# Kernel tuning notes

Measured on AMD Instinct MI355X. Metric: run time of the kernel, lower is better.

The kernel has to match this reference:

```python
import jax, jax.numpy as jnp
import numpy as np

H = 2048      # hidden_size
I = 4096      # intermediate_size
N = 128       # ssm state_size
HEADS = 64
P = 64        # head_dim
K = 4         # conv kernel
CHUNK = 256
DT_MIN, DT_MAX = 0.0, 100.0
EPS = 1e-5


def segsum(x):
    # x: (..., T) -> (..., T, T) with out[i, j] = sum_{k=j+1..i} x[k], -inf above diag
    T = x.shape[-1]
    cs = jnp.cumsum(x, axis=-1)
    d = cs[..., :, None] - cs[..., None, :]
    mask = jnp.tril(jnp.ones((T, T), dtype=bool))
    return jnp.where(mask, d, -jnp.inf)


def setup_inputs() -> dict:
    key = jax.random.key(0)
    ks = jax.random.split(key, 8)
    return {
        "hidden_states": jax.random.normal(ks[0], (2, 4096, H), jnp.float32),
        "in_proj_w": jax.random.normal(ks[1], (2 * (I + N) + HEADS, H), jnp.float32) * 0.02,
        "conv_w": jax.random.normal(ks[2], (I + 2 * N, 1, K), jnp.float32) * 0.2,
        "conv_b": jax.random.normal(ks[3], (I + 2 * N,), jnp.float32) * 0.02,
        "dt_bias": jax.random.uniform(ks[4], (HEADS,), jnp.float32),
        "A_log": jnp.log(jax.random.uniform(ks[5], (HEADS,), jnp.float32, 1.0, 16.0)),
        "D": jnp.ones((HEADS,), jnp.float32),
        "norm_w": jnp.ones((I,), jnp.float32),
        "out_proj_w": jax.random.normal(ks[6], (H, I), jnp.float32) * 0.02,
    }


def reference(hidden_states, in_proj_w, conv_w, conv_b, dt_bias, A_log, D, norm_w, out_proj_w):
    b, l, _ = hidden_states.shape
    # in_proj -> [z (I), xBC (I+2N), dt (HEADS)]  (d_mlp == 0 with these dims)
    zxbcdt = hidden_states @ in_proj_w.T
    z, xBC, dt = jnp.split(zxbcdt, [I, I + (I + 2 * N)], axis=-1)

    # causal depthwise conv1d + SiLU
    conv = jax.lax.conv_general_dilated(
        xBC.transpose(0, 2, 1), conv_w, (1,), [(K - 1, 0)],
        dimension_numbers=("NCH", "OIH", "NCH"), feature_group_count=I + 2 * N)
    xBC = jax.nn.silu((conv + conv_b[None, :, None]).transpose(0, 2, 1))
    x, B, C = jnp.split(xBC, [I, I + N], axis=-1)

    A = -jnp.exp(A_log)                                        # (h,)
    dt = jnp.clip(jax.nn.softplus(dt + dt_bias), DT_MIN, DT_MAX)  # (b,l,h)

    # SSD chunked scan (groups = 1 for B/C)
    X = x.reshape(b, l, HEADS, P) * dt[..., None]              # x * dt
    Adt = dt * A                                               # (b,l,h)
    c = l // CHUNK
    Xc = X.reshape(b, c, CHUNK, HEADS, P)
    Bc = B.reshape(b, c, CHUNK, N)
    Cc = C.reshape(b, c, CHUNK, N)
    Ac = Adt.reshape(b, c, CHUNK, HEADS).transpose(0, 3, 1, 2)  # (b,h,c,cl)
    A_cum = jnp.cumsum(Ac, axis=-1)

    # intra-chunk (diagonal) contribution
    L = jnp.exp(segsum(Ac))                                    # (b,h,c,cl,cl)
    Y_diag = jnp.einsum("bcln,bcsn,bhcls,bcshp->bclhp", Cc, Bc, L, Xc)

    # chunk states and inter-chunk recurrence
    decay_states = jnp.exp(A_cum[..., -1:] - A_cum)            # (b,h,c,cl)
    states = jnp.einsum("bcln,bhcl,bclhp->bchpn", Bc, decay_states, Xc)
    states = jnp.concatenate([jnp.zeros_like(states[:, :1]), states], axis=1)
    chunk_A = jnp.pad(A_cum[..., -1], ((0, 0), (0, 0), (1, 0)))  # (b,h,c+1)
    decay_chunk = jnp.exp(segsum(chunk_A))                     # (b,h,c+1,c+1)
    new_states = jnp.einsum("bhzc,bchpn->bzhpn", decay_chunk, states)
    prev_states = new_states[:, :-1]                           # (b,c,h,p,n)

    Y_off = jnp.einsum("bcln,bchpn,bhcl->bclhp", Cc, prev_states, jnp.exp(A_cum))
    y = (Y_diag + Y_off).reshape(b, l, HEADS, P)
    y = y + x.reshape(b, l, HEADS, P) * D[None, None, :, None]  # skip (D term)
    y = y.reshape(b, l, I)

    # gated RMSNorm (norm_before_gate=True): normalize, gate by silu(z), scale
    yf = y.astype(jnp.float32)
    yf = yf * jax.lax.rsqrt(jnp.mean(yf * yf, axis=-1, keepdims=True) + EPS)
    yf = yf * jax.nn.silu(z.astype(jnp.float32))
    y = (norm_w * yf).astype(hidden_states.dtype)

    return y @ out_proj_w.T
```

## Files before the change

### kernel.cpp

```cpp
#include <hip/hip_runtime.h>

typedef unsigned short u16;
typedef __attribute__((ext_vector_type(8))) short bfx8;
typedef __attribute__((ext_vector_type(4))) float f32x4;
typedef __attribute__((ext_vector_type(4))) unsigned short u16x4;

__device__ __forceinline__ float bf2f(u16 u){ return __builtin_bit_cast(float, (unsigned)u << 16); }
__device__ __forceinline__ u16 f2bf(float f){
  unsigned u = __builtin_bit_cast(unsigned, f);
  return (u16)((u + 0x7fffu + ((u >> 16) & 1u)) >> 16);
}

__device__ __forceinline__ void gload_lds16(const void* g, void* l){
  __builtin_amdgcn_global_load_lds((const __attribute__((address_space(1))) void*)g,
                                   (__attribute__((address_space(3))) void*)l, 16, 0, 0);
}

__global__ __launch_bounds__(256) void cvt_kernel(const float* __restrict__ in, u16* __restrict__ out, int n4){
  int i = blockIdx.x * 256 + threadIdx.x;
  if (i >= n4) return;
  f32x4 v = *(const f32x4*)&in[(long)i * 4];
  u16x4 o = { f2bf(v[0]), f2bf(v[1]), f2bf(v[2]), f2bf(v[3]) };
  *(u16x4*)&out[(long)i * 4] = o;
}

template<int F32OUT>
__global__ __launch_bounds__(512, 2)
void gemm256(const u16* __restrict__ A, const u16* __restrict__ W,
             void* __restrict__ out0, void* __restrict__ out1,
             int K, int ld0, int ld1, int nsplit)
{
  __shared__ __align__(16) u16 SA[2][16384];
  __shared__ __align__(16) u16 SB[2][16384];
  const int tid = threadIdx.x;
  const int wid = tid >> 6, lane = tid & 63;
  const int wr = wid >> 2, wc = wid & 3;
  const int bm = blockIdx.x, bn = blockIdx.y;
  const int rr = lane & 15, kg = lane >> 4;
  const int NT = K >> 6;

  const int srow = tid >> 3;
  const int ssw = ((tid & 7) * 16) ^ ((srow & 7) << 4);
  const u16* gA = A + ((long)bm * 256 + srow) * K + (ssw >> 1);
  const u16* gB = W + ((long)bn * 256 + srow) * K + (ssw >> 1);
  const long r64 = (long)64 * K;
  const int dst = tid * 8;

#define STAGE_A(t, ht) { const u16* s_ = gA + (long)(ht) * 2 * r64 + ((t) << 6); \
    gload_lds16(s_,       &SA[(t) & 1][(ht) * 8192 + dst]); \
    gload_lds16(s_ + r64, &SA[(t) & 1][(ht) * 8192 + 4096 + dst]); }
#define STAGE_B(t, ht) { const u16* s_ = gB + (long)(ht) * 2 * r64 + ((t) << 6); \
    gload_lds16(s_,       &SB[(t) & 1][(ht) * 8192 + dst]); \
    gload_lds16(s_ + r64, &SB[(t) & 1][(ht) * 8192 + 4096 + dst]); }

  const int swr = (rr & 7) << 4;
  const int ca0 = ((kg * 16) ^ swr) >> 1;
  const int ca1 = ((64 + kg * 16) ^ swr) >> 1;
  int bA[8], bB[4];
#pragma unroll
  for (int j = 0; j < 8; j++) bA[j] = ((2 * j + wr) * 16 + rr) * 64;
#pragma unroll
  for (int i = 0; i < 4; i++) bB[i] = ((4 * i + wc) * 16 + rr) * 64;

  f32x4 acc[8][4] = {};

  STAGE_A(0, 0); STAGE_A(0, 1); STAGE_B(0, 0); STAGE_B(0, 1);
  if (NT > 1) STAGE_A(1, 0);
  asm volatile("s_waitcnt vmcnt(2)" ::: "memory");
  asm volatile("s_barrier" ::: "memory");

  for (int u = 0; u < NT; ++u){
    const int p = u & 1;
    bfx8 bf[4][2];
#pragma unroll
    for (int k = 0; k < 4; ++k){
      bfx8 af[2][2];
#pragma unroll
      for (int jj = 0; jj < 2; jj++){
        const int base = bA[2 * k + jj];
        af[jj][0] = *(const bfx8*)&SA[p][base + ca0];
        af[jj][1] = *(const bfx8*)&SA[p][base + ca1];
      }
      if (k == 0){
#pragma unroll
        for (int i = 0; i < 4; i++){
          bf[i][0] = *(const bfx8*)&SB[p][bB[i] + ca0];
          bf[i][1] = *(const bfx8*)&SB[p][bB[i] + ca1];
        }
        if (u + 1 < NT) { STAGE_B(u + 1, 0); STAGE_B(u + 1, 1); }
      }
      else if (k == 1) { if (u + 1 < NT) STAGE_A(u + 1, 1); }
      else if (k == 3) {
        if (u + 2 < NT)      { STAGE_A(u + 2, 0); asm volatile("s_waitcnt vmcnt(2)" ::: "memory"); }
        else if (u + 1 < NT) { asm volatile("s_waitcnt vmcnt(0)" ::: "memory"); }
      }
      asm volatile("s_barrier" ::: "memory");
      __builtin_amdgcn_s_setprio(1);
#pragma unroll
      for (int jj = 0; jj < 2; jj++)
#pragma unroll
        for (int i = 0; i < 4; i++){
          acc[2 * k + jj][i] = __builtin_amdgcn_mfma_f32_16x16x32_bf16(af[jj][0], bf[i][0], acc[2 * k + jj][i], 0, 0, 0);
          acc[2 * k + jj][i] = __builtin_amdgcn_mfma_f32_16x16x32_bf16(af[jj][1], bf[i][1], acc[2 * k + jj][i], 0, 0, 0);
        }
      __builtin_amdgcn_s_setprio(0);
    }
  }
#undef STAGE_A
#undef STAGE_B

  int bn2 = bn; void* op = out0; int ldo = ld0;
  if (bn >= nsplit){ bn2 = bn - nsplit; op = out1; ldo = ld1; }
  const int r4b = (lane >> 4) * 4;
#pragma unroll
  for (int j = 0; j < 8; j++)
#pragma unroll
    for (int i = 0; i < 4; i++)
#pragma unroll
      for (int r4 = 0; r4 < 4; r4++){
        long row = (long)bm * 256 + (2 * j + wr) * 16 + r4b + r4;
        long col = (long)bn2 * 256 + (4 * i + wc) * 16 + rr;
        long idx = row * ldo + col;
        if (F32OUT) ((float*)op)[idx] = acc[j][i][r4];
        else        ((u16*)op)[idx]  = f2bf(acc[j][i][r4]);
      }
}

__global__ __launch_bounds__(256) void dt_kernel(const float* __restrict__ hs, const float* __restrict__ w,
                                                 const float* __restrict__ dt_bias, float* __restrict__ dtp){
  __shared__ float hsS[32][66];
  __shared__ float wS[64][66];
  const int tid = threadIdx.x;
  const int j = tid & 63, rgrp = tid >> 6;
  const long row0 = (long)blockIdx.x * 32;
  const int srow = tid >> 3, sc0 = (tid & 7) * 8;
  const int wrow = tid >> 2, wc0 = (tid & 3) * 16;
  const float* hsg = hs + (row0 + srow) * 2048 + sc0;
  const float* wg  = w + (long)(8448 + wrow) * 2048 + wc0;

  f32x4 acc[8] = {};
  for (int k0 = 0; k0 < 2048; k0 += 64){
    *(f32x4*)&hsS[srow][sc0]     = *(const f32x4*)&hsg[k0];
    *(f32x4*)&hsS[srow][sc0 + 4] = *(const f32x4*)&hsg[k0 + 4];
#pragma unroll
    for (int q = 0; q < 4; q++)
      *(f32x4*)&wS[wrow][wc0 + q * 4] = *(const f32x4*)&wg[k0 + q * 4];
    __syncthreads();
#pragma unroll
    for (int kk = 0; kk < 64; kk += 4){
      f32x4 wv = *(const f32x4*)&wS[j][kk];
#pragma unroll
      for (int r = 0; r < 8; r++){
        f32x4 hv = *(const f32x4*)&hsS[rgrp * 8 + r][kk];
        acc[r] += hv * wv;
      }
    }
    __syncthreads();
  }
  float bias = dt_bias[j];
#pragma unroll
  for (int r = 0; r < 8; r++){
    float x = acc[r][0] + acc[r][1] + acc[r][2] + acc[r][3] + bias;
    float sp = (x > 20.f) ? x : log1pf(expf(x));
    sp = fminf(fmaxf(sp, 0.f), 100.f);
    dtp[(row0 + rgrp * 8 + r) * 64 + j] = sp;
  }
}

__global__ __launch_bounds__(64) void acum_kernel(const float* __restrict__ dtp, const float* __restrict__ A_log,
                                                  float* __restrict__ acum, float* __restrict__ suma){
  int bid = blockIdx.x;
  int c = bid & 15, h = (bid >> 4) & 63, b = bid >> 10;
  int lane = threadIdx.x;
  float Ah = -expf(A_log[h]);
  long base = ((long)(b * 4096 + c * 256)) * 64 + h;
  float v[4]; float s = 0.f;
#pragma unroll
  for (int i = 0; i < 4; i++){ float adt = dtp[base + (lane * 4 + i) * 64] * Ah; s += adt; v[i] = s; }
  float tot = s, run = s;
  for (int off = 1; off < 64; off <<= 1){ float u = __shfl_up(run, off); if (lane >= off) run += u; }
  float excl = run - tot;
  long ob = (long)bid * 256 + lane * 4;
#pragma unroll
  for (int i = 0; i < 4; i++) acum[ob + i] = excl + v[i];
  if (lane == 63) suma[bid] = run;
}

__global__ __launch_bounds__(256) void conv_kernel(const u16* __restrict__ xbc, const float* __restrict__ cw,
                                                   const float* __restrict__ cb,
                                                   u16* __restrict__ xact,
                                                   u16* __restrict__ bmat, u16* __restrict__ cmat){
  int pos = blockIdx.x;
  int l = pos & 4095;
  for (int cg = threadIdx.x; cg < 544; cg += 256){
    int ch = cg * 8;
    f32x4 cwv[8];
#pragma unroll
    for (int t = 0; t < 8; t++) cwv[t] = *(const f32x4*)&cw[(ch + t) * 4];
    float acc[8];
#pragma unroll
    for (int t = 0; t < 8; t++) acc[t] = cb[ch + t];
#pragma unroll
    for (int k = 0; k < 4; k++){
      int lp = l + k - 3;
      if (lp < 0) continue;
      bfx8 xv = *(const bfx8*)&xbc[(long)(pos + k - 3) * 4352 + ch];
#pragma unroll
      for (int t = 0; t < 8; t++) acc[t] += cwv[t][k] * bf2f((u16)xv[t]);
    }
    bfx8 o;
#pragma unroll
    for (int t = 0; t < 8; t++){
      float val = acc[t] / (1.f + expf(-acc[t]));
      o[t] = (short)f2bf(val);
    }
    if (ch < 4096)      *(bfx8*)&xact[(long)pos * 4096 + ch] = o;
    else if (ch < 4224) *(bfx8*)&bmat[(long)pos * 128 + ch - 4096] = o;
    else                *(bfx8*)&cmat[(long)pos * 128 + ch - 4224] = o;
  }
}

__global__ __launch_bounds__(256) void bt_transpose(const u16* __restrict__ bmat, u16* __restrict__ bmatT){
  __shared__ u16 T[128 * 136];
  int bx = blockIdx.x;
  int b = bx >> 5, lt = bx & 31;
  int l0 = lt * 128;
  int tid = threadIdx.x;
  for (int idx = tid; idx < 2048; idx += 256){
    int lrow = idx >> 4, ns = (idx & 15) * 8;
    *(bfx8*)&T[lrow * 136 + ns] = *(const bfx8*)&bmat[((long)b * 4096 + l0 + lrow) * 128 + ns];
  }
  __syncthreads();
  for (int idx = tid; idx < 2048; idx += 256){
    int nrow = idx >> 4, ls = (idx & 15) * 8;
    bfx8 o;
#pragma unroll
    for (int j = 0; j < 8; j++) o[j] = (short)T[(ls + j) * 136 + nrow];
    *(bfx8*)&bmatT[(long)b * 524288 + (long)nrow * 4096 + l0 + ls] = o;
  }
}

__global__ __launch_bounds__(256, 4) void states_kernel(const u16* __restrict__ xact, const u16* __restrict__ bmatT,
                                                        const float* __restrict__ acum, const float* __restrict__ suma,
                                                        const float* __restrict__ dtp, u16* __restrict__ stR){
  __shared__ __align__(16) u16 XdT[64 * 264];
  __shared__ float fac[256];
  int bid = blockIdx.x;
  int h = bid & 63, c = (bid >> 6) & 15, b = bid >> 10;
  int tid = threadIdx.x;
  long rowbase = (long)b * 4096 + c * 256;
  long aco = ((long)((b * 64 + h) * 16 + c)) * 256;
  float sA = suma[(b * 64 + h) * 16 + c];
  fac[tid] = dtp[(rowbase + tid) * 64 + h] * expf(sA - acum[aco + tid]);
  __syncthreads();
  for (int idx = tid; idx < 2048; idx += 256){
    int l = idx >> 3, ps = (idx & 7) * 8;
    bfx8 xv = *(const bfx8*)&xact[(rowbase + l) * 4096 + h * 64 + ps];
#pragma unroll
    for (int j = 0; j < 8; j++)
      XdT[(ps + j) * 264 + l] = f2bf(bf2f((u16)xv[j]) * fac[l]);
  }
  __syncthreads();
  int wid = tid >> 6, lane = tid & 63;
  int rr = lane & 15, ko = (lane >> 4) * 8;
  const u16* btb = bmatT + (long)b * 524288 + c * 256;
  f32x4 acc[8] = {};
#pragma unroll
  for (int ks = 0; ks < 8; ks++){
    bfx8 a = *(const bfx8*)&XdT[(wid * 16 + rr) * 264 + ks * 32 + ko];
#pragma unroll
    for (int nt = 0; nt < 8; nt++){
      bfx8 bb = *(const bfx8*)&btb[(long)(nt * 16 + rr) * 4096 + ks * 32 + ko];
      acc[nt] = __builtin_amdgcn_mfma_f32_16x16x32_bf16(a, bb, acc[nt], 0, 0, 0);
    }
  }
  long ob = (long)bid * 8192;
#pragma unroll
  for (int nt = 0; nt < 8; nt++)
#pragma unroll
    for (int r4 = 0; r4 < 4; r4++){
      int p = wid * 16 + (lane >> 4) * 4 + r4;
      stR[ob + p * 128 + nt * 16 + rr] = f2bf(acc[nt][r4]);
    }
}

__global__ __launch_bounds__(256) void scan_kernel(u16* stR, const float* __restrict__ suma){
  int g = blockIdx.x;
  int s = g & 7, bh = g >> 3;
  int b = bh >> 6, h = bh & 63;
  int tid = threadIdx.x;
  long off0 = (long)s * 1024 + tid * 4;
  f32x4 R = {};
  for (int c = 0; c < 16; c++){
    long base = ((long)((b * 16 + c) * 64 + h)) * 8192 + off0;
    float sc = expf(suma[(b * 64 + h) * 16 + c]);
    u16x4 e4 = *(const u16x4*)&stR[base];
    u16x4 o = { f2bf(R[0]), f2bf(R[1]), f2bf(R[2]), f2bf(R[3]) };
    *(u16x4*)&stR[base] = o;
#pragma unroll
    for (int t = 0; t < 4; t++) R[t] = sc * R[t] + bf2f(e4[t]);
  }
}

__global__ __launch_bounds__(256, 3) void ydiag_kernel(const u16* __restrict__ cmat, const u16* __restrict__ bmat,
                                                       const u16* xact,
                                                       const u16* __restrict__ rbuf, const float* __restrict__ acum,
                                                       const float* __restrict__ dtp,
                                                       const float* __restrict__ Dv, u16* ybuf){
  __shared__ __align__(16) u16 XdTq[64 * 72];
  __shared__ __align__(16) u16 Sb[4][64 * 36];
  __shared__ float acL[256];
  __shared__ float dtl[256];
  int bid = blockIdx.x;
  int h = bid & 63, c = (bid >> 6) & 15, b = bid >> 10;
  int tid = threadIdx.x, wid = tid >> 6, lane = tid & 63;
  long rowbase = (long)b * 4096 + c * 256;
  long aco = ((long)((b * 64 + h) * 16 + c)) * 256;
  acL[tid] = acum[aco + tid];
  dtl[tid] = dtp[(rowbase + tid) * 64 + h];
  __syncthreads();

  int rr = lane & 15, ko = (lane >> 4) * 8;
  f32x4 acc[4][4] = {};

  long rb = (long)bid * 8192;
#pragma unroll
  for (int kk = 0; kk < 4; kk++){
    bfx8 cf[4];
#pragma unroll
    for (int lt = 0; lt < 4; lt++)
      cf[lt] = *(const bfx8*)&cmat[(rowbase + wid * 64 + lt * 16 + rr) * 128 + kk * 32 + ko];
#pragma unroll
    for (int pt = 0; pt < 4; pt++){
      bfx8 bb = *(const bfx8*)&rbuf[rb + (pt * 16 + rr) * 128 + kk * 32 + ko];
#pragma unroll
      for (int lt = 0; lt < 4; lt++) acc[lt][pt] = __builtin_amdgcn_mfma_f32_16x16x32_bf16(cf[lt], bb, acc[lt][pt], 0, 0, 0);
    }
  }
#pragma unroll
  for (int lt = 0; lt < 4; lt++)
#pragma unroll
    for (int r4 = 0; r4 < 4; r4++){
      float e = expf(acL[wid * 64 + lt * 16 + (lane >> 4) * 4 + r4]);
#pragma unroll
      for (int pt = 0; pt < 4; pt++) acc[lt][pt][r4] *= e;
    }

  const int nsp = 2 * (wid + 1);
  for (int q = 0; q < 4; q++){
    __syncthreads();
    for (int idx = tid; idx < 512; idx += 256){
      int lq = idx >> 3, ps = (idx & 7) * 8;
      int l = q * 64 + lq;
      bfx8 xv = *(const bfx8*)&xact[(rowbase + l) * 4096 + h * 64 + ps];
#pragma unroll
      for (int j = 0; j < 8; j++)
        XdTq[(ps + j) * 72 + lq] = f2bf(bf2f((u16)xv[j]) * dtl[l]);
    }
    __syncthreads();
#pragma unroll
    for (int sub = 0; sub < 2; sub++){
      int sp = q * 2 + sub;
      if (sp >= nsp) continue;
      int s0 = sp * 32;
      f32x4 sacc[2][4] = {};
#pragma unroll
      for (int kk = 0; kk < 4; kk++){
        bfx8 cf[4];
#pragma unroll
        for (int lt = 0; lt < 4; lt++)
          cf[lt] = *(const bfx8*)&cmat[(rowbase + wid * 64 + lt * 16 + rr) * 128 + kk * 32 + ko];
#pragma unroll
        for (int st = 0; st < 2; st++){
          bfx8 bb = *(const bfx8*)&bmat[(rowbase + s0 + st * 16 + rr) * 128 + kk * 32 + ko];
#pragma unroll
          for (int lt = 0; lt < 4; lt++) sacc[st][lt] = __builtin_amdgcn_mfma_f32_16x16x32_bf16(cf[lt], bb, sacc[st][lt], 0, 0, 0);
        }
      }
#pragma unroll
      for (int st = 0; st < 2; st++)
#pragma unroll
        for (int lt = 0; lt < 4; lt++)
#pragma unroll
          for (int r4 = 0; r4 < 4; r4++){
            int lrow = wid * 64 + lt * 16 + (lane >> 4) * 4 + r4;
            int scol = s0 + st * 16 + rr;
            float vv = (scol <= lrow) ? sacc[st][lt][r4] * expf(acL[lrow] - acL[scol]) : 0.f;
            Sb[wid][(lt * 16 + (lane >> 4) * 4 + r4) * 36 + st * 16 + rr] = f2bf(vv);
          }
      asm volatile("s_waitcnt lgkmcnt(0)" ::: "memory");
      __builtin_amdgcn_sched_barrier(0);
#pragma unroll
      for (int lt = 0; lt < 4; lt++){
        bfx8 a1 = *(const bfx8*)&Sb[wid][(lt * 16 + rr) * 36 + ko];
#pragma unroll
        for (int pt = 0; pt < 4; pt++){
          bfx8 bb = *(const bfx8*)&XdTq[(pt * 16 + rr) * 72 + sub * 32 + ko];
          acc[lt][pt] = __builtin_amdgcn_mfma_f32_16x16x32_bf16(a1, bb, acc[lt][pt], 0, 0, 0);
        }
      }
    }
  }
  float Dh = Dv[h];
#pragma unroll
  for (int lt = 0; lt < 4; lt++)
#pragma unroll
    for (int pt = 0; pt < 4; pt++)
#pragma unroll
      for (int r4 = 0; r4 < 4; r4++){
        int lrow = wid * 64 + lt * 16 + (lane >> 4) * 4 + r4;
        int pcol = pt * 16 + rr;
        long gi = (rowbase + lrow) * 4096 + h * 64 + pcol;
        ybuf[gi] = f2bf(acc[lt][pt][r4] + bf2f(xact[gi]) * Dh);
      }
}

__global__ __launch_bounds__(256) void rms_kernel(const u16* ybuf, const u16* zbuf,
                                                  const float* __restrict__ norm_w, u16* ynorm){
  __shared__ float red[4];
  long row = blockIdx.x;
  int tid = threadIdx.x;
  long yb = row * 4096 + tid * 16;
  bfx8 v0 = *(const bfx8*)&ybuf[yb];
  bfx8 v1 = *(const bfx8*)&ybuf[yb + 8];
  float vals[16];
#pragma unroll
  for (int t = 0; t < 8; t++){ vals[t] = bf2f((u16)v0[t]); vals[8 + t] = bf2f((u16)v1[t]); }
  float ss = 0.f;
#pragma unroll
  for (int t = 0; t < 16; t++) ss += vals[t] * vals[t];
#pragma unroll
  for (int off = 32; off >= 1; off >>= 1) ss += __shfl_xor(ss, off);
  if ((tid & 63) == 0) red[tid >> 6] = ss;
  __syncthreads();
  float rs = rsqrtf((red[0] + red[1] + red[2] + red[3]) * (1.f / 4096.f) + 1e-5f);
  bfx8 z0 = *(const bfx8*)&zbuf[yb];
  bfx8 z1 = *(const bfx8*)&zbuf[yb + 8];
  bfx8 o0, o1;
#pragma unroll
  for (int t = 0; t < 16; t++){
    float zv = bf2f((u16)(t < 8 ? z0[t] : z1[t - 8]));
    float g = zv / (1.f + expf(-zv));
    u16 r = f2bf(vals[t] * rs * norm_w[tid * 16 + t] * g);
    if (t < 8) o0[t] = (short)r; else o1[t - 8] = (short)r;
  }
  *(bfx8*)&ynorm[yb] = o0;
  *(bfx8*)&ynorm[yb + 8] = o1;
}

extern "C" void kernel_launch(void* const* d_in, const int* in_sizes, int n_in,
                              void* d_out, int out_size, void* d_ws, size_t ws_size,
                              hipStream_t stream){
  const float* hs   = (const float*)d_in[0];
  const float* inw  = (const float*)d_in[1];
  const float* cw   = (const float*)d_in[2];
  const float* cb   = (const float*)d_in[3];
  const float* dtb  = (const float*)d_in[4];
  const float* alog = (const float*)d_in[5];
  const float* Dv   = (const float*)d_in[6];
  const float* nw   = (const float*)d_in[7];
  const float* outw = (const float*)d_in[8];

  const size_t REQ = 147857408ULL;
  if (ws_size < REQ){
    hipMemsetAsync(d_out, 0x42, (size_t)out_size * 4, stream);
    return;
  }
  char* ws = (char*)d_ws;
  u16*   hsb  = (u16*)  (ws + 0L);
  u16*   wbi  = (u16*)  (ws + 33554432L);
  u16*   xbc  = (u16*)  (ws + 68157440L);
  u16*   xact = (u16*)  (ws + 0L);
  u16*   stR  = (u16*)  (ws + 68157440L);
  u16*   wbo  = (u16*)  (ws + 101711872L);
  u16*   bmatT= (u16*)  (ws + 118489088L);
  float* dtp  = (float*)(ws + 139460608L);
  float* acum = (float*)(ws + 141557760L);
  float* suma = (float*)(ws + 143654912L);
  u16*   bmat = (u16*)  (ws + 143663104L);
  u16*   cmat = (u16*)  (ws + 145760256L);
  u16*   zbuf = (u16*)  d_out;

  cvt_kernel<<<16384, 256, 0, stream>>>(hs, hsb, 4194304);
  cvt_kernel<<<16896, 256, 0, stream>>>(inw, wbi, 4325376);
  gemm256<0><<<dim3(32, 33), 512, 0, stream>>>(hsb, wbi, zbuf, xbc, 2048, 4096, 4352, 16);
  dt_kernel<<<256, 256, 0, stream>>>(hs, inw, dtb, dtp);
  acum_kernel<<<2048, 64, 0, stream>>>(dtp, alog, acum, suma);
  conv_kernel<<<8192, 256, 0, stream>>>(xbc, cw, cb, xact, bmat, cmat);
  cvt_kernel<<<8192, 256, 0, stream>>>(outw, wbo, 2097152);
  bt_transpose<<<64, 256, 0, stream>>>(bmat, bmatT);
  states_kernel<<<2048, 256, 0, stream>>>(xact, bmatT, acum, suma, dtp, stR);
  scan_kernel<<<1024, 256, 0, stream>>>(stR, suma);
  ydiag_kernel<<<2048, 256, 0, stream>>>(cmat, bmat, xact, stR, acum, dtp, Dv, xact);
  rms_kernel<<<8192, 256, 0, stream>>>(xact, zbuf, nw, xact);
  gemm256<1><<<dim3(32, 8), 512, 0, stream>>>(xact, wbo, d_out, d_out, 4096, 2048, 2048, 999);
}
```

Baseline: 1.033 ms.

## Software-pipeline GEMM LDS reads, merge cvt launches, and reuse conv inputs across positions

The GEMM main loop now prefetches the next A and B fragments from LDS while the current MFMA phase runs, and is unrolled by two tiles so the buffer index is a compile-time constant. The two fp32-to-bf16 conversion launches are merged into one kernel to save a launch. The conv kernel now handles four sequence positions per block and keeps a 7-row sliding window in registers, so each input row is loaded about once per channel group instead of four times. Risks are higher register pressure in the GEMM at 2 blocks per SM, and the two-tile unroll assumes NT is even, which holds for K=2048 and K=4096.

```diff
diff --git a/kernel.cpp b/kernel.cpp
--- a/kernel.cpp
+++ b/kernel.cpp
@@ -22,6 +22,17 @@
   f32x4 v = *(const f32x4*)&in[(long)i * 4];
   u16x4 o = { f2bf(v[0]), f2bf(v[1]), f2bf(v[2]), f2bf(v[3]) };
   *(u16x4*)&out[(long)i * 4] = o;
+}
+
+__global__ __launch_bounds__(256) void cvt2_kernel(const float* __restrict__ a, u16* __restrict__ oa, int na4,
+                                                   const float* __restrict__ b2, u16* __restrict__ ob, int nb4){
+  int i = blockIdx.x * 256 + threadIdx.x;
+  const float* src; u16* dst; int idx;
+  if (i < na4){ src = a; dst = oa; idx = i; }
+  else { idx = i - na4; if (idx >= nb4) return; src = b2; dst = ob; }
+  f32x4 v = *(const f32x4*)&src[(long)idx * 4];
+  u16x4 o = { f2bf(v[0]), f2bf(v[1]), f2bf(v[2]), f2bf(v[3]) };
+  *(u16x4*)&dst[(long)idx * 4] = o;
 }
 
 template<int F32OUT>
@@ -63,49 +74,64 @@
   for (int i = 0; i < 4; i++) bB[i] = ((4 * i + wc) * 16 + rr) * 64;
 
   f32x4 acc[8][4] = {};
+  bfx8 af[2][2], bf[4][2];
+
+#define RD_AF(P, F0) { \
+    af[0][0] = *(const bfx8*)&SA[P][bA[F0] + ca0];     af[0][1] = *(const bfx8*)&SA[P][bA[F0] + ca1]; \
+    af[1][0] = *(const bfx8*)&SA[P][bA[(F0)+1] + ca0]; af[1][1] = *(const bfx8*)&SA[P][bA[(F0)+1] + ca1]; }
+#define RD_BF(P) { \
+    _Pragma("unroll") \
+    for (int i = 0; i < 4; i++){ \
+      bf[i][0] = *(const bfx8*)&SB[P][bB[i] + ca0]; bf[i][1] = *(const bfx8*)&SB[P][bB[i] + ca1]; } }
+#define PHASE_MFMA(KK) { \
+    __builtin_amdgcn_s_setprio(1); \
+    _Pragma("unroll") \
+    for (int jj = 0; jj < 2; jj++) \
+      _Pragma("unroll") \
+      for (int i = 0; i < 4; i++){ \
+        acc[2*(KK)+jj][i] = __builtin_amdgcn_mfma_f32_16x16x32_bf16(af[jj][0], bf[i][0], acc[2*(KK)+jj][i], 0, 0, 0); \
+        acc[2*(KK)+jj][i] = __builtin_amdgcn_mfma_f32_16x16x32_bf16(af[jj][1], bf[i][1], acc[2*(KK)+jj][i], 0, 0, 0); \
+      } \
+    __builtin_amdgcn_s_setprio(0); }
+
+#define TILE(u, P) { \
+     \
+    if ((u) + 1 < NT){ STAGE_B((u) + 1, 0); STAGE_B((u) + 1, 1); } \
+    asm volatile("s_barrier" ::: "memory"); \
+    PHASE_MFMA(0); \
+    RD_AF(P, 2); \
+     \
+    if ((u) + 1 < NT){ STAGE_A((u) + 1, 1); } \
+    asm volatile("s_barrier" ::: "memory"); \
+    PHASE_MFMA(1); \
+    RD_AF(P, 4); \
+     \
+    asm volatile("s_barrier" ::: "memory"); \
+    PHASE_MFMA(2); \
+    RD_AF(P, 6); \
+     \
+    if ((u) + 2 < NT){ STAGE_A((u) + 2, 0); asm volatile("s_waitcnt vmcnt(2)" ::: "memory"); } \
+    else if ((u) + 1 < NT){ asm volatile("s_waitcnt vmcnt(0)" ::: "memory"); } \
+    asm volatile("s_barrier" ::: "memory"); \
+    PHASE_MFMA(3); \
+    if ((u) + 1 < NT){ RD_AF((P) ^ 1, 0); RD_BF((P) ^ 1); } \
+  }
 
   STAGE_A(0, 0); STAGE_A(0, 1); STAGE_B(0, 0); STAGE_B(0, 1);
   if (NT > 1) STAGE_A(1, 0);
   asm volatile("s_waitcnt vmcnt(2)" ::: "memory");
   asm volatile("s_barrier" ::: "memory");
-
-  for (int u = 0; u < NT; ++u){
-    const int p = u & 1;
-    bfx8 bf[4][2];
-#pragma unroll
-    for (int k = 0; k < 4; ++k){
-      bfx8 af[2][2];
-#pragma unroll
-      for (int jj = 0; jj < 2; jj++){
-        const int base = bA[2 * k + jj];
-        af[jj][0] = *(const bfx8*)&SA[p][base + ca0];
-        af[jj][1] = *(const bfx8*)&SA[p][base + ca1];
-      }
-      if (k == 0){
-#pragma unroll
-        for (int i = 0; i < 4; i++){
-          bf[i][0] = *(const bfx8*)&SB[p][bB[i] + ca0];
-          bf[i][1] = *(const bfx8*)&SB[p][bB[i] + ca1];
-        }
-        if (u + 1 < NT) { STAGE_B(u + 1, 0); STAGE_B(u + 1, 1); }
-      }
-      else if (k == 1) { if (u + 1 < NT) STAGE_A(u + 1, 1); }
-      else if (k == 3) {
-        if (u + 2 < NT)      { STAGE_A(u + 2, 0); asm volatile("s_waitcnt vmcnt(2)" ::: "memory"); }
-        else if (u + 1 < NT) { asm volatile("s_waitcnt vmcnt(0)" ::: "memory"); }
-      }
-      asm volatile("s_barrier" ::: "memory");
-      __builtin_amdgcn_s_setprio(1);
-#pragma unroll
-      for (int jj = 0; jj < 2; jj++)
-#pragma unroll
-        for (int i = 0; i < 4; i++){
-          acc[2 * k + jj][i] = __builtin_amdgcn_mfma_f32_16x16x32_bf16(af[jj][0], bf[i][0], acc[2 * k + jj][i], 0, 0, 0);
-          acc[2 * k + jj][i] = __builtin_amdgcn_mfma_f32_16x16x32_bf16(af[jj][1], bf[i][1], acc[2 * k + jj][i], 0, 0, 0);
-        }
-      __builtin_amdgcn_s_setprio(0);
-    }
-  }
+  RD_AF(0, 0);
+  RD_BF(0);
+
+  for (int uu = 0; uu < NT; uu += 2){
+    TILE(uu, 0);
+    TILE(uu + 1, 1);
+  }
+#undef TILE
+#undef PHASE_MFMA
+#undef RD_BF
+#undef RD_AF
 #undef STAGE_A
 #undef STAGE_B
 
@@ -190,33 +216,39 @@
                                                    const float* __restrict__ cb,
                                                    u16* __restrict__ xact,
                                                    u16* __restrict__ bmat, u16* __restrict__ cmat){
-  int pos = blockIdx.x;
-  int l = pos & 4095;
+  int pb = blockIdx.x;
+  int l0 = (pb & 1023) * 4;
+  long pos0 = ((long)(pb >> 10) << 12) + l0;
   for (int cg = threadIdx.x; cg < 544; cg += 256){
     int ch = cg * 8;
     f32x4 cwv[8];
 #pragma unroll
     for (int t = 0; t < 8; t++) cwv[t] = *(const f32x4*)&cw[(ch + t) * 4];
-    float acc[8];
-#pragma unroll
-    for (int t = 0; t < 8; t++) acc[t] = cb[ch + t];
-#pragma unroll
-    for (int k = 0; k < 4; k++){
-      int lp = l + k - 3;
-      if (lp < 0) continue;
-      bfx8 xv = *(const bfx8*)&xbc[(long)(pos + k - 3) * 4352 + ch];
-#pragma unroll
-      for (int t = 0; t < 8; t++) acc[t] += cwv[t][k] * bf2f((u16)xv[t]);
-    }
-    bfx8 o;
-#pragma unroll
-    for (int t = 0; t < 8; t++){
-      float val = acc[t] / (1.f + expf(-acc[t]));
-      o[t] = (short)f2bf(val);
-    }
-    if (ch < 4096)      *(bfx8*)&xact[(long)pos * 4096 + ch] = o;
-    else if (ch < 4224) *(bfx8*)&bmat[(long)pos * 128 + ch - 4096] = o;
-    else                *(bfx8*)&cmat[(long)pos * 128 + ch - 4224] = o;
+    float cbv[8];
+#pragma unroll
+    for (int t = 0; t < 8; t++) cbv[t] = cb[ch + t];
+    bfx8 rr[7];
+    bfx8 zz = {};
+    rr[0] = (l0 >= 3) ? *(const bfx8*)&xbc[(pos0 - 3) * 4352 + ch] : zz;
+    rr[1] = (l0 >= 2) ? *(const bfx8*)&xbc[(pos0 - 2) * 4352 + ch] : zz;
+    rr[2] = (l0 >= 1) ? *(const bfx8*)&xbc[(pos0 - 1) * 4352 + ch] : zz;
+#pragma unroll
+    for (int q = 0; q < 4; q++) rr[3 + q] = *(const bfx8*)&xbc[(pos0 + q) * 4352 + ch];
+#pragma unroll
+    for (int li = 0; li < 4; li++){
+      bfx8 o;
+#pragma unroll
+      for (int t = 0; t < 8; t++){
+        float a = cbv[t] + cwv[t][0] * bf2f((u16)rr[li][t])     + cwv[t][1] * bf2f((u16)rr[li + 1][t])
+                         + cwv[t][2] * bf2f((u16)rr[li + 2][t]) + cwv[t][3] * bf2f((u16)rr[li + 3][t]);
+        float val = a / (1.f + expf(-a));
+        o[t] = (short)f2bf(val);
+      }
+      long pos = pos0 + li;
+      if (ch < 4096)      *(bfx8*)&xact[pos * 4096 + ch] = o;
+      else if (ch < 4224) *(bfx8*)&bmat[pos * 128 + ch - 4096] = o;
+      else                *(bfx8*)&cmat[pos * 128 + ch - 4224] = o;
+    }
   }
 }
 
@@ -481,12 +513,11 @@
   u16*   cmat = (u16*)  (ws + 145760256L);
   u16*   zbuf = (u16*)  d_out;
 
-  cvt_kernel<<<16384, 256, 0, stream>>>(hs, hsb, 4194304);
-  cvt_kernel<<<16896, 256, 0, stream>>>(inw, wbi, 4325376);
+  cvt2_kernel<<<33280, 256, 0, stream>>>(hs, hsb, 4194304, inw, wbi, 4325376);
   gemm256<0><<<dim3(32, 33), 512, 0, stream>>>(hsb, wbi, zbuf, xbc, 2048, 4096, 4352, 16);
   dt_kernel<<<256, 256, 0, stream>>>(hs, inw, dtb, dtp);
   acum_kernel<<<2048, 64, 0, stream>>>(dtp, alog, acum, suma);
-  conv_kernel<<<8192, 256, 0, stream>>>(xbc, cw, cb, xact, bmat, cmat);
+  conv_kernel<<<2048, 256, 0, stream>>>(xbc, cw, cb, xact, bmat, cmat);
   cvt_kernel<<<8192, 256, 0, stream>>>(outw, wbo, 2097152);
   bt_transpose<<<64, 256, 0, stream>>>(bmat, bmatT);
   states_kernel<<<2048, 256, 0, stream>>>(xact, bmatT, acum, suma, dtp, stR);
```

Result: no change. 1.017 ms (-1.5%).
